# Kernel optimization log

Hardware: AMD Instinct MI355X
Metric: run time of the kernel (lower is better)

## Reference

```python
import jax, jax.numpy as jnp
import numpy as np

B, KEY, D, U, MODES = 16384, 64, 128, 128, 32

def setup_inputs() -> dict:
    key = jax.random.key(0)
    k1, k2, k3, k4, k5 = jax.random.split(key, 5)
    return {
        "key": jax.random.normal(k1, (B, KEY), dtype=jnp.float32),
        "x": jax.random.normal(k2, (B, D), dtype=jnp.float32),
        "sens": jnp.ones((MODES,), dtype=jnp.float32),
        "keys_map": jax.random.normal(k3, (MODES, KEY), dtype=jnp.float32),
        "kernels": jax.random.normal(k4, (MODES, D, U), dtype=jnp.float32) * 0.05,
        "biases": jax.random.normal(k5, (MODES, U), dtype=jnp.float32) * 0.05,
    }

def reference(key, x, sens, keys_map, kernels, biases):
    # key: [B, KEY]; keys_map: [MODES, KEY]
    # Euclidean distance of each key to each mode's stored key.
    dist = jnp.sqrt(jnp.sum((key[:, None, :] - keys_map[None, :, :]) ** 2, axis=-1))  # [B, MODES]
    sim = jax.nn.softmax(sens / (dist + 1.0), axis=-1)  # [B, MODES]
    modes = kernels.shape[0]
    # Original: kernel_b = mean_m(sim[b,m] * kernels[m]); out_b = x_b @ kernel_b.
    # Reordered as GEMM-per-mode + weighted combine (same math):
    out = jnp.einsum('bm,bd,mdu->bu', sim, x, kernels) / modes  # [B, U]
    out = out + (sim @ biases) / modes  # mean over modes of sim-weighted biases
    return out
```

## Files before the change

### kernel.cpp

```cpp
#include <hip/hip_runtime.h>

#define BATCH 16384
#define KEYD  64
#define DDIM  128
#define UDIM  128
#define MODES 32

typedef __attribute__((ext_vector_type(8))) short bf16x8;
typedef __attribute__((ext_vector_type(4))) float f32x4;

__device__ __forceinline__ unsigned short f2bf(float f) {
  unsigned u = __float_as_uint(f);
  unsigned r = (u + 0x7FFFu + ((u >> 16) & 1u)) >> 16;
  return (unsigned short)r;
}

__device__ __forceinline__ void gld_lds16(const void* g, void* l) {
  __builtin_amdgcn_global_load_lds(
      (const __attribute__((address_space(1))) unsigned int*)g,
      (__attribute__((address_space(3))) unsigned int*)l, 16, 0, 0);
}

__global__ __launch_bounds__(256) void prep_all(
    const float* __restrict__ key, const float* __restrict__ x,
    const float* __restrict__ sens, const float* __restrict__ keys_map,
    const float* __restrict__ kernels, const float* __restrict__ biases,
    float* __restrict__ sim, unsigned short* __restrict__ x16,
    unsigned short* __restrict__ kb16, unsigned short* __restrict__ bb16) {
  const int t = threadIdx.x;
  const int bid = blockIdx.x;

  if (bid < BATCH / 32) {
    __shared__ float kr[32][KEYD];
    *(float4*)(&kr[0][0] + t * 4) =
        *(const float4*)(key + (long)bid * 32 * KEYD + t * 4);
    *(float4*)(&kr[0][0] + 1024 + t * 4) =
        *(const float4*)(key + (long)bid * 32 * KEYD + 1024 + t * 4);

    const int lane = t & 63, wave = t >> 6;
    const int m = lane & 31, h = lane >> 5;
    float kreg[32];
    {
      const float* kmp = keys_map + m * KEYD + h * 32;
      #pragma unroll
      for (int j = 0; j < 32; j += 4) {
        const float4 v = *(const float4*)(kmp + j);
        kreg[j] = v.x; kreg[j + 1] = v.y; kreg[j + 2] = v.z; kreg[j + 3] = v.w;
      }
    }
    const float sv = sens[m];
    __syncthreads();

    #pragma unroll
    for (int rr = 0; rr < 8; ++rr) {
      const int rl = wave * 8 + rr;
      const long row = (long)bid * 32 + rl;

      float d2h = 0.f;
      #pragma unroll
      for (int j = 0; j < 32; j += 2) {
        const float2 kv = *(const float2*)(&kr[rl][h * 32 + j]);
        float a = kv.x - kreg[j], b = kv.y - kreg[j + 1];
        d2h += a * a + b * b;
      }
      float d2 = d2h + __shfl_xor(d2h, 32, 64);
      float logit = sv / (sqrtf(d2) + 1.0f);
      float mx = logit;
      #pragma unroll
      for (int off = 16; off > 0; off >>= 1) mx = fmaxf(mx, __shfl_xor(mx, off, 64));
      float e = __expf(logit - mx);
      float s = e;
      #pragma unroll
      for (int off = 16; off > 0; off >>= 1) s += __shfl_xor(s, off, 64);
      if (h == 0) sim[row * MODES + m] = e / s;

      const float2 xv = *(const float2*)(x + row * DDIM + lane * 2);
      ushort2 o; o.x = f2bf(xv.x); o.y = f2bf(xv.y);
      *(ushort2*)(x16 + row * DDIM + lane * 2) = o;
    }
  } else {
    int tt = (bid - BATCH / 32) * 256 + t;
    if (tt < MODES * 16 * UDIM) {
      int u = tt & 127, kb = (tt >> 7) & 15, m = tt >> 11;
      const float* src = kernels + (long)((m * 16 + kb) * 8) * UDIM + u;
      ushort4 lo, hi;
      lo.x = f2bf(src[0 * UDIM]); lo.y = f2bf(src[1 * UDIM]);
      lo.z = f2bf(src[2 * UDIM]); lo.w = f2bf(src[3 * UDIM]);
      hi.x = f2bf(src[4 * UDIM]); hi.y = f2bf(src[5 * UDIM]);
      hi.z = f2bf(src[6 * UDIM]); hi.w = f2bf(src[7 * UDIM]);
      *(ushort4*)(kb16 + (long)tt * 8) = lo;
      *(ushort4*)(kb16 + (long)tt * 8 + 4) = hi;
    } else {
      int tb = tt - MODES * 16 * UDIM;
      int u = tb & 127, kb = tb >> 7;
      const float* src = biases + kb * 8 * UDIM + u;
      ushort4 lo, hi;
      lo.x = f2bf(src[0 * UDIM]); lo.y = f2bf(src[1 * UDIM]);
      lo.z = f2bf(src[2 * UDIM]); lo.w = f2bf(src[3 * UDIM]);
      hi.x = f2bf(src[4 * UDIM]); hi.y = f2bf(src[5 * UDIM]);
      hi.z = f2bf(src[6 * UDIM]); hi.w = f2bf(src[7 * UDIM]);
      *(ushort4*)(bb16 + (long)tb * 8) = lo;
      *(ushort4*)(bb16 + (long)tb * 8 + 4) = hi;
    }
  }
}

__global__ __launch_bounds__(256, 2) void gemm_poly(
    const unsigned short* __restrict__ x16, const unsigned short* __restrict__ kb16,
    const unsigned short* __restrict__ bb16, const float* __restrict__ sim,
    float* __restrict__ partial) {
  __shared__ alignas(16) unsigned short bsh[2][16 * UDIM * 8];
  __shared__ alignas(16) float simT[8][128];

  const int t = threadIdx.x;
  const int lane = t & 63, w = t >> 6;
  const int q = lane >> 4, l16 = lane & 15;
  const int wrow = (w >> 1) * 64, wcol = (w & 1) * 64;
  const long bm = (long)blockIdx.x * 128;
  const int split = blockIdx.y;

  {
    int rrow = t >> 1, mg = (t & 1) * 4;
    const float4 v = *(const float4*)(sim + (bm + rrow) * MODES + split * 8 + mg);
    simT[mg + 0][rrow] = v.x; simT[mg + 1][rrow] = v.y;
    simT[mg + 2][rrow] = v.z; simT[mg + 3][rrow] = v.w;
  }

  bf16x8 aF[4][4];
  #pragma unroll
  for (int rt = 0; rt < 4; ++rt)
    #pragma unroll
    for (int ks = 0; ks < 4; ++ks)
      aF[rt][ks] = *(const bf16x8*)(x16 + (bm + wrow + rt * 16 + l16) * DDIM + ks * 32 + q * 8);

  const unsigned short* kbase = kb16 + (long)(split * 8) * (16 * UDIM * 8);
  #pragma unroll
  for (int i = 0; i < 8; ++i) {
    int off = (t + i * 256) * 8;
    gld_lds16(kbase + off, &bsh[0][off]);
  }

  f32x4 acc[4][4] = {};

  for (int mi = 0; mi < 8; ++mi) {
    __syncthreads();
    if (mi < 7) {
      const unsigned short* src = kbase + (long)(mi + 1) * (16 * UDIM * 8);
      unsigned short* dst = bsh[(mi + 1) & 1];
      #pragma unroll
      for (int i = 0; i < 8; ++i) {
        int off = (t + i * 256) * 8;
        gld_lds16(src + off, dst + off);
      }
    }

    const unsigned short* bs = bsh[mi & 1];
    bf16x8 bF[4][4];
    #pragma unroll
    for (int ks = 0; ks < 4; ++ks)
      #pragma unroll
      for (int ct = 0; ct < 4; ++ct)
        bF[ks][ct] = *(const bf16x8*)&bs[(((ks * 4 + q) * UDIM) + wcol + ct * 16 + l16) * 8];

    #pragma unroll
    for (int rt = 0; rt < 4; ++rt) {
      f32x4 tmp[4] = {};
      #pragma unroll
      for (int ks = 0; ks < 4; ++ks)
        #pragma unroll
        for (int ct = 0; ct < 4; ++ct)
          tmp[ct] = __builtin_amdgcn_mfma_f32_16x16x32_bf16(aF[rt][ks], bF[ks][ct], tmp[ct], 0, 0, 0);
      const f32x4 s = *(const f32x4*)&simT[mi][wrow + rt * 16 + q * 4];
      #pragma unroll
      for (int ct = 0; ct < 4; ++ct)
        acc[rt][ct] += s * tmp[ct];
    }
  }

  if (split == 0) {
    bf16x8 sF[4];
    #pragma unroll
    for (int rt = 0; rt < 4; ++rt) {
      const float* sp = sim + (bm + wrow + rt * 16 + l16) * MODES + q * 8;
      bf16x8 f;
      #pragma unroll
      for (int j = 0; j < 8; ++j) f[j] = (short)f2bf(sp[j]);
      sF[rt] = f;
    }
    #pragma unroll
    for (int ct = 0; ct < 4; ++ct) {
      bf16x8 bb = *(const bf16x8*)(bb16 + (long)(q * UDIM + wcol + ct * 16 + l16) * 8);
      #pragma unroll
      for (int rt = 0; rt < 4; ++rt)
        acc[rt][ct] = __builtin_amdgcn_mfma_f32_16x16x32_bf16(sF[rt], bb, acc[rt][ct], 0, 0, 0);
    }
  }

  float* part = partial + (long)split * ((long)BATCH * UDIM);
  #pragma unroll
  for (int rt = 0; rt < 4; ++rt)
    #pragma unroll
    for (int ct = 0; ct < 4; ++ct) {
      long row = bm + wrow + rt * 16 + q * 4;
      int col = wcol + ct * 16 + l16;
      #pragma unroll
      for (int r = 0; r < 4; ++r)
        part[(row + r) * UDIM + col] = acc[rt][ct][r];
    }
}

__global__ __launch_bounds__(256) void reduce_parts(
    const float* __restrict__ partial, float* __restrict__ out) {
  const long i = ((long)blockIdx.x * 256 + threadIdx.x) * 4;
  const long S = (long)BATCH * UDIM;
  const f32x4 p0 = *(const f32x4*)(partial + i);
  const f32x4 p1 = *(const f32x4*)(partial + S + i);
  const f32x4 p2 = *(const f32x4*)(partial + 2 * S + i);
  const f32x4 p3 = *(const f32x4*)(partial + 3 * S + i);
  *(f32x4*)(out + i) = (p0 + p1 + p2 + p3) * (1.0f / MODES);
}

extern "C" void kernel_launch(void* const* d_in, const int* in_sizes, int n_in,
                              void* d_out, int out_size, void* d_ws, size_t ws_size,
                              hipStream_t stream) {
  const float* key      = (const float*)d_in[0];
  const float* x        = (const float*)d_in[1];
  const float* sens     = (const float*)d_in[2];
  const float* keys_map = (const float*)d_in[3];
  const float* kernels  = (const float*)d_in[4];
  const float* biases   = (const float*)d_in[5];
  float* out = (float*)d_out;

  char* ws = (char*)d_ws;
  float*          sim  = (float*)ws;
  unsigned short* x16  = (unsigned short*)(ws + (2u << 20));
  unsigned short* kb16 = (unsigned short*)(ws + (6u << 20));
  unsigned short* bb16 = (unsigned short*)(ws + (7u << 20));
  float*          part = (float*)(ws + (8u << 20));

  prep_all<<<BATCH / 32 + 258, 256, 0, stream>>>(
      key, x, sens, keys_map, kernels, biases, sim, x16, kb16, bb16);
  gemm_poly<<<dim3(BATCH / 128, 4), 256, 0, stream>>>(x16, kb16, bb16, sim, part);
  reduce_parts<<<(BATCH * UDIM) / (256 * 4), 256, 0, stream>>>(part, out);
}
```

Before: 107.6 us.

## Fuse mode split and reduction into one GEMM kernel with direct register B loads

The GEMM kernel stops splitting the 32 modes across four blocks, which wrote fp32 partials that a separate reduce kernel summed. Each block now covers 64 rows by 64 columns and loops over all 32 modes. Each wave reads its B fragments straight from global memory into registers with a two-deep prefetch, replacing the LDS staging and barriers. This removes the partial-buffer traffic and one kernel launch. In exchange, per-block work is serial across modes and B reuse drops, since every wave fetches its own B slice from global memory or L2.

```diff
diff --git a/kernel.cpp b/kernel.cpp
--- a/kernel.cpp
+++ b/kernel.cpp
@@ -13,12 +13,6 @@
   unsigned u = __float_as_uint(f);
   unsigned r = (u + 0x7FFFu + ((u >> 16) & 1u)) >> 16;
   return (unsigned short)r;
-}
-
-__device__ __forceinline__ void gld_lds16(const void* g, void* l) {
-  __builtin_amdgcn_global_load_lds(
-      (const __attribute__((address_space(1))) unsigned int*)g,
-      (__attribute__((address_space(3))) unsigned int*)l, 16, 0, 0);
 }
 
 __global__ __launch_bounds__(256) void prep_all(
@@ -105,25 +99,55 @@
   }
 }
 
-__global__ __launch_bounds__(256, 2) void gemm_poly(
+#define MODE_STRIDE (16 * UDIM * 8)
+
+#define MODE_STEP(MI, CUR, NXT, PREFETCH)                                       \
+  {                                                                             \
+    if (PREFETCH) {                                                             \
+      _Pragma("unroll")                                                         \
+      for (int ks = 0; ks < 4; ++ks)                                            \
+        NXT[ks] = *(const bf16x8*)(pM + (long)((MI) + 1) * MODE_STRIDE +        \
+                                   ks * (4 * UDIM * 8));                        \
+    }                                                                           \
+    f32x4 tmp0 = {}, tmp1 = {}, tmp2 = {}, tmp3 = {};                           \
+    _Pragma("unroll")                                                           \
+    for (int ks = 0; ks < 4; ++ks) {                                            \
+      tmp0 = __builtin_amdgcn_mfma_f32_16x16x32_bf16(aF[0][ks], CUR[ks], tmp0, 0, 0, 0); \
+      tmp1 = __builtin_amdgcn_mfma_f32_16x16x32_bf16(aF[1][ks], CUR[ks], tmp1, 0, 0, 0); \
+      tmp2 = __builtin_amdgcn_mfma_f32_16x16x32_bf16(aF[2][ks], CUR[ks], tmp2, 0, 0, 0); \
+      tmp3 = __builtin_amdgcn_mfma_f32_16x16x32_bf16(aF[3][ks], CUR[ks], tmp3, 0, 0, 0); \
+    }                                                                           \
+    {                                                                           \
+      const f32x4 s0 = *(const f32x4*)&simT[MI][0 * 16 + q * 4];                \
+      const f32x4 s1 = *(const f32x4*)&simT[MI][1 * 16 + q * 4];                \
+      const f32x4 s2 = *(const f32x4*)&simT[MI][2 * 16 + q * 4];                \
+      const f32x4 s3 = *(const f32x4*)&simT[MI][3 * 16 + q * 4];                \
+      acc[0] += s0 * tmp0; acc[1] += s1 * tmp1;                                 \
+      acc[2] += s2 * tmp2; acc[3] += s3 * tmp3;                                 \
+    }                                                                           \
+  }
+
+__global__ __launch_bounds__(256, 2) void gemm_direct(
     const unsigned short* __restrict__ x16, const unsigned short* __restrict__ kb16,
     const unsigned short* __restrict__ bb16, const float* __restrict__ sim,
-    float* __restrict__ partial) {
-  __shared__ alignas(16) unsigned short bsh[2][16 * UDIM * 8];
-  __shared__ alignas(16) float simT[8][128];
+    float* __restrict__ out) {
+  __shared__ float simT[MODES][64];
 
   const int t = threadIdx.x;
   const int lane = t & 63, w = t >> 6;
   const int q = lane >> 4, l16 = lane & 15;
-  const int wrow = (w >> 1) * 64, wcol = (w & 1) * 64;
-  const long bm = (long)blockIdx.x * 128;
-  const int split = blockIdx.y;
+  const long bm = (long)blockIdx.x * 64;
+  const int ch = blockIdx.y;
+  const int ucol = ch * 64 + w * 16 + l16;
 
   {
-    int rrow = t >> 1, mg = (t & 1) * 4;
-    const float4 v = *(const float4*)(sim + (bm + rrow) * MODES + split * 8 + mg);
-    simT[mg + 0][rrow] = v.x; simT[mg + 1][rrow] = v.y;
-    simT[mg + 2][rrow] = v.z; simT[mg + 3][rrow] = v.w;
+    const int r = t >> 2, mg = (t & 3) * 8;
+    const float4 v0 = *(const float4*)(sim + (bm + r) * MODES + mg);
+    const float4 v1 = *(const float4*)(sim + (bm + r) * MODES + mg + 4);
+    simT[mg + 0][r] = v0.x; simT[mg + 1][r] = v0.y;
+    simT[mg + 2][r] = v0.z; simT[mg + 3][r] = v0.w;
+    simT[mg + 4][r] = v1.x; simT[mg + 5][r] = v1.y;
+    simT[mg + 6][r] = v1.z; simT[mg + 7][r] = v1.w;
   }
 
   bf16x8 aF[4][4];
@@ -131,93 +155,46 @@
   for (int rt = 0; rt < 4; ++rt)
     #pragma unroll
     for (int ks = 0; ks < 4; ++ks)
-      aF[rt][ks] = *(const bf16x8*)(x16 + (bm + wrow + rt * 16 + l16) * DDIM + ks * 32 + q * 8);
-
-  const unsigned short* kbase = kb16 + (long)(split * 8) * (16 * UDIM * 8);
+      aF[rt][ks] = *(const bf16x8*)(x16 + (bm + rt * 16 + l16) * DDIM + ks * 32 + q * 8);
+
+  const unsigned short* pM = kb16 + ((long)q * UDIM + ucol) * 8;
+
+  __syncthreads();
+
+  f32x4 acc[4] = {};
+  bf16x8 bA[4], bB[4];
   #pragma unroll
-  for (int i = 0; i < 8; ++i) {
-    int off = (t + i * 256) * 8;
-    gld_lds16(kbase + off, &bsh[0][off]);
-  }
-
-  f32x4 acc[4][4] = {};
-
-  for (int mi = 0; mi < 8; ++mi) {
-    __syncthreads();
-    if (mi < 7) {
-      const unsigned short* src = kbase + (long)(mi + 1) * (16 * UDIM * 8);
-      unsigned short* dst = bsh[(mi + 1) & 1];
-      #pragma unroll
-      for (int i = 0; i < 8; ++i) {
-        int off = (t + i * 256) * 8;
-        gld_lds16(src + off, dst + off);
-      }
-    }
-
-    const unsigned short* bs = bsh[mi & 1];
-    bf16x8 bF[4][4];
-    #pragma unroll
-    for (int ks = 0; ks < 4; ++ks)
-      #pragma unroll
-      for (int ct = 0; ct < 4; ++ct)
-        bF[ks][ct] = *(const bf16x8*)&bs[(((ks * 4 + q) * UDIM) + wcol + ct * 16 + l16) * 8];
-
+  for (int ks = 0; ks < 4; ++ks)
+    bA[ks] = *(const bf16x8*)(pM + ks * (4 * UDIM * 8));
+
+  for (int mi = 0; mi < MODES; mi += 2) {
+    MODE_STEP(mi, bA, bB, true);
+    MODE_STEP(mi + 1, bB, bA, (mi + 2 < MODES));
+  }
+
+  {
+    const bf16x8 bb = *(const bf16x8*)(bb16 + ((long)q * UDIM + ucol) * 8);
     #pragma unroll
     for (int rt = 0; rt < 4; ++rt) {
-      f32x4 tmp[4] = {};
-      #pragma unroll
-      for (int ks = 0; ks < 4; ++ks)
-        #pragma unroll
-        for (int ct = 0; ct < 4; ++ct)
-          tmp[ct] = __builtin_amdgcn_mfma_f32_16x16x32_bf16(aF[rt][ks], bF[ks][ct], tmp[ct], 0, 0, 0);
-      const f32x4 s = *(const f32x4*)&simT[mi][wrow + rt * 16 + q * 4];
-      #pragma unroll
-      for (int ct = 0; ct < 4; ++ct)
-        acc[rt][ct] += s * tmp[ct];
-    }
-  }
-
-  if (split == 0) {
-    bf16x8 sF[4];
-    #pragma unroll
-    for (int rt = 0; rt < 4; ++rt) {
-      const float* sp = sim + (bm + wrow + rt * 16 + l16) * MODES + q * 8;
-      bf16x8 f;
-      #pragma unroll
-      for (int j = 0; j < 8; ++j) f[j] = (short)f2bf(sp[j]);
-      sF[rt] = f;
-    }
-    #pragma unroll
-    for (int ct = 0; ct < 4; ++ct) {
-      bf16x8 bb = *(const bf16x8*)(bb16 + (long)(q * UDIM + wcol + ct * 16 + l16) * 8);
-      #pragma unroll
-      for (int rt = 0; rt < 4; ++rt)
-        acc[rt][ct] = __builtin_amdgcn_mfma_f32_16x16x32_bf16(sF[rt], bb, acc[rt][ct], 0, 0, 0);
-    }
-  }
-
-  float* part = partial + (long)split * ((long)BATCH * UDIM);
+      const float* sp = sim + (bm + rt * 16 + l16) * MODES + q * 8;
+      const float4 sv0 = *(const float4*)(sp);
+      const float4 sv1 = *(const float4*)(sp + 4);
+      bf16x8 sF;
+      sF[0] = (short)f2bf(sv0.x); sF[1] = (short)f2bf(sv0.y);
+      sF[2] = (short)f2bf(sv0.z); sF[3] = (short)f2bf(sv0.w);
+      sF[4] = (short)f2bf(sv1.x); sF[5] = (short)f2bf(sv1.y);
+      sF[6] = (short)f2bf(sv1.z); sF[7] = (short)f2bf(sv1.w);
+      acc[rt] = __builtin_amdgcn_mfma_f32_16x16x32_bf16(sF, bb, acc[rt], 0, 0, 0);
+    }
+  }
+
   #pragma unroll
-  for (int rt = 0; rt < 4; ++rt)
-    #pragma unroll
-    for (int ct = 0; ct < 4; ++ct) {
-      long row = bm + wrow + rt * 16 + q * 4;
-      int col = wcol + ct * 16 + l16;
-      #pragma unroll
-      for (int r = 0; r < 4; ++r)
-        part[(row + r) * UDIM + col] = acc[rt][ct][r];
-    }
-}
-
-__global__ __launch_bounds__(256) void reduce_parts(
-    const float* __restrict__ partial, float* __restrict__ out) {
-  const long i = ((long)blockIdx.x * 256 + threadIdx.x) * 4;
-  const long S = (long)BATCH * UDIM;
-  const f32x4 p0 = *(const f32x4*)(partial + i);
-  const f32x4 p1 = *(const f32x4*)(partial + S + i);
-  const f32x4 p2 = *(const f32x4*)(partial + 2 * S + i);
-  const f32x4 p3 = *(const f32x4*)(partial + 3 * S + i);
-  *(f32x4*)(out + i) = (p0 + p1 + p2 + p3) * (1.0f / MODES);
+  for (int rt = 0; rt < 4; ++rt) {
+    const long row = bm + rt * 16 + q * 4;
+    #pragma unroll
+    for (int r = 0; r < 4; ++r)
+      out[(row + r) * UDIM + ucol] = acc[rt][r] * (1.0f / MODES);
+  }
 }
 
 extern "C" void kernel_launch(void* const* d_in, const int* in_sizes, int n_in,
@@ -236,10 +213,8 @@
   unsigned short* x16  = (unsigned short*)(ws + (2u << 20));
   unsigned short* kb16 = (unsigned short*)(ws + (6u << 20));
   unsigned short* bb16 = (unsigned short*)(ws + (7u << 20));
-  float*          part = (float*)(ws + (8u << 20));
 
   prep_all<<<BATCH / 32 + 258, 256, 0, stream>>>(
       key, x, sens, keys_map, kernels, biases, sim, x16, kb16, bb16);
-  gemm_poly<<<dim3(BATCH / 128, 4), 256, 0, stream>>>(x16, kb16, bb16, sim, part);
-  reduce_parts<<<(BATCH * UDIM) / (256 * 4), 256, 0, stream>>>(part, out);
-}
+  gemm_direct<<<dim3(BATCH / 64, 2), 256, 0, stream>>>(x16, kb16, bb16, sim, out);
+}
```

Measured after the change: 157.5 us. +46.3%, slower.
